# Kernel optimization log

Hardware: AMD Instinct MI355X
Metric: run time of the kernel (lower is better)

Reference implementation:

```python
import jax, jax.numpy as jnp
import numpy as np

B, NI, H, NC = 524288, 32, 128, 64


def _masks(ni, h):
    deg_in = jnp.arange(ni)                     # input layer: arange % ni == arange
    deg_hid = jnp.arange(h) % (ni - 1)
    deg_out = jnp.arange(2 * ni) % ni - 1
    m1 = (deg_hid[:, None] >= deg_in[None, :]).astype(jnp.float32)   # [H, NI]
    m2 = (deg_hid[:, None] >= deg_hid[None, :]).astype(jnp.float32)  # [H, H]
    m3 = (deg_out[:, None] >= deg_hid[None, :]).astype(jnp.float32)  # [2NI, H]
    return m1, m2, m3


def setup_inputs() -> dict:
    key = jax.random.key(0)
    ks = jax.random.split(key, 9)
    s = 0.05
    return {
        "x": jax.random.normal(ks[0], (B, NI), jnp.float32),
        "cond": jax.random.normal(ks[1], (B, NC), jnp.float32),
        "W1": jax.random.normal(ks[2], (H, NI), jnp.float32) * s,
        "b1": jnp.zeros((H,), jnp.float32),
        "Wc": jax.random.normal(ks[3], (H, NC), jnp.float32) * s,
        "W2": jax.random.normal(ks[4], (H, H), jnp.float32) * s,
        "b2": jnp.zeros((H,), jnp.float32),
        "W3": jax.random.normal(ks[5], (2 * NI, H), jnp.float32) * s,
        "b3": jnp.zeros((2 * NI,), jnp.float32),
    }


def reference(x, cond, W1, b1, Wc, W2, b2, W3, b3):
    ni = x.shape[1]
    h_dim = W1.shape[0]
    m1, m2, m3 = _masks(ni, h_dim)
    # joiner: masked linear + conditioning linear (no bias on cond)
    h = x @ (W1 * m1).T + b1 + cond @ Wc.T            # [B, H]
    h = jax.nn.relu(h)
    h = jax.nn.relu(h @ (W2 * m2).T + b2)             # [B, H]
    o = h @ (W3 * m3).T + b3                          # [B, 2NI]
    m_, a = o[:, :ni], o[:, ni:]
    a = jnp.clip(a, -5.0, 5.0)
    u = (x - m_) * jnp.exp(-a)
    logdet = -jnp.sum(a, axis=-1, keepdims=True)
    return u, logdet
```

## Files before the change

kernel.cpp:

```cpp
#include <hip/hip_runtime.h>


#define B_ROWS 524288
#define NI 32
#define HD 128
#define NC 64
#define ITERS 4

#define L2_BASE 24
#define L3_BASE 56
#define N_FRAGS 72

typedef _Float16 half8 __attribute__((ext_vector_type(8)));
typedef float f32x4 __attribute__((ext_vector_type(4)));

__device__ inline f32x4 relu4(f32x4 v) {
  v[0] = fmaxf(v[0], 0.f); v[1] = fmaxf(v[1], 0.f);
  v[2] = fmaxf(v[2], 0.f); v[3] = fmaxf(v[3], 0.f);
  return v;
}

__device__ inline half8 cvt8(f32x4 lo, f32x4 hi) {
  half8 h;
  h[0] = (_Float16)lo[0]; h[1] = (_Float16)lo[1];
  h[2] = (_Float16)lo[2]; h[3] = (_Float16)lo[3];
  h[4] = (_Float16)hi[0]; h[5] = (_Float16)hi[1];
  h[6] = (_Float16)hi[2]; h[7] = (_Float16)hi[3];
  return h;
}

__global__ void prep_weights(const float* __restrict__ W1, const float* __restrict__ Wc,
                             const float* __restrict__ W2, const float* __restrict__ W3,
                             _Float16* __restrict__ wf) {
  int tid = blockIdx.x * blockDim.x + threadIdx.x;
  if (tid >= N_FRAGS * 64) return;
  int frag = tid >> 6;
  int lane = tid & 63;
  int q = lane >> 4, c = lane & 15;
  int L, jt, kt;
  if (frag < L2_BASE)      { L = 0; jt = frag / 3;              kt = frag % 3; }
  else if (frag < L3_BASE) { L = 1; jt = (frag - L2_BASE) >> 2; kt = (frag - L2_BASE) & 3; }
  else                     { L = 2; jt = (frag - L3_BASE) >> 2; kt = (frag - L3_BASE) & 3; }
  int j = jt * 16 + c;
  half8 v;
#pragma unroll
  for (int e = 0; e < 8; ++e) {
    int k = kt * 32 + (e >> 2) * 16 + q * 4 + (e & 3);
    float w;
    if (L == 0) {
      if (k < NI) w = ((j % 31) >= k) ? W1[j * NI + k] : 0.f;
      else        w = Wc[j * NC + (k - NI)];
    } else if (L == 1) {
      w = ((j % 31) >= (k % 31)) ? W2[j * HD + k] : 0.f;
    } else {
      w = (((j % 32) - 1) >= (k % 31)) ? W3[j * HD + k] : 0.f;
    }
    v[e] = (_Float16)w;
  }
  *(half8*)(wf + (size_t)tid * 8) = v;
}


#define BODY(RX, RC, NRX, NRC, IT, SYNC)                                      \
  {                                                                           \
    half8 bf0 = cvt8(RX[0], RX[1]);                                           \
    half8 bf1 = cvt8(RC[0], RC[1]);                                           \
    half8 bf2 = cvt8(RC[2], RC[3]);                                           \
    if ((IT) < ITERS - 1) {     \
      long nr = blockBase + ((IT) + 1) * 128 + wid * 16 + c;                  \
      const f32x4* xr = (const f32x4*)(x + nr * NI);                          \
      const f32x4* cr = (const f32x4*)(cond + nr * NC);                       \
      NRX[0] = xr[q];     NRX[1] = xr[4 + q];                                 \
      NRC[0] = cr[q];     NRC[1] = cr[4 + q];                                 \
      NRC[2] = cr[8 + q]; NRC[3] = cr[12 + q];                                \
    }                                                                         \
    f32x4 acc[4]; half8 h1[4], h2[4];                                         \
          \
    _Pragma("unroll")                                                         \
    for (int jh = 0; jh < 2; ++jh) {                                          \
      _Pragma("unroll")                                                       \
      for (int j4 = 0; j4 < 4; ++j4)                                          \
        acc[j4] = *(const f32x4*)(b1 + (jh * 4 + j4) * 16 + q * 4);           \
      _Pragma("unroll")                                                       \
      for (int j4 = 0; j4 < 4; ++j4) {                                        \
        int jt = jh * 4 + j4;                                                 \
        _Pragma("unroll")                                                     \
        for (int kt = 0; kt < 3; ++kt) {                                      \
          half8 a = *(const half8*)(wf + (((jt * 3 + kt) * 64 + lane) << 3)); \
          half8 bb = (kt == 0) ? bf0 : ((kt == 1) ? bf1 : bf2);               \
          acc[j4] = __builtin_amdgcn_mfma_f32_16x16x32_f16(a, bb, acc[j4], 0, 0, 0); \
        }                                                                     \
      }                                                                       \
      _Pragma("unroll")                                                       \
      for (int p = 0; p < 2; ++p)                                             \
        h1[jh * 2 + p] = cvt8(relu4(acc[p * 2]), relu4(acc[p * 2 + 1]));      \
    }                                                                         \
    if (SYNC) __syncthreads();           \
                           \
    _Pragma("unroll")                                                         \
    for (int jh = 0; jh < 2; ++jh) {                                          \
      _Pragma("unroll")                                                       \
      for (int j4 = 0; j4 < 4; ++j4)                                          \
        acc[j4] = *(const f32x4*)(b2 + (jh * 4 + j4) * 16 + q * 4);           \
      _Pragma("unroll")                                                       \
      for (int j4 = 0; j4 < 4; ++j4) {                                        \
        int jt = jh * 4 + j4;                                                 \
        _Pragma("unroll")                                                     \
        for (int kt = 0; kt < 4; ++kt) {                                      \
          half8 a = *(const half8*)(wlds + (((jt * 4 + kt) * 64 + lane) << 3)); \
          acc[j4] = __builtin_amdgcn_mfma_f32_16x16x32_f16(a, h1[kt], acc[j4], 0, 0, 0); \
        }                                                                     \
      }                                                                       \
      _Pragma("unroll")                                                       \
      for (int p = 0; p < 2; ++p)                                             \
        h2[jh * 2 + p] = cvt8(relu4(acc[p * 2]), relu4(acc[p * 2 + 1]));      \
    }                                                                         \
                \
    _Pragma("unroll")                                                         \
    for (int jt = 0; jt < 4; ++jt)                                            \
      acc[jt] = *(const f32x4*)(b3 + jt * 16 + q * 4);                        \
    _Pragma("unroll")                                                         \
    for (int jt = 0; jt < 4; ++jt) {                                          \
      _Pragma("unroll")                                                       \
      for (int kt = 0; kt < 4; ++kt) {                                        \
        half8 a = *(const half8*)(wlds + (((32 + jt * 4 + kt) * 64 + lane) << 3)); \
        acc[jt] = __builtin_amdgcn_mfma_f32_16x16x32_f16(a, h2[kt], acc[jt], 0, 0, 0); \
      }                                                                       \
    }                                                                         \
                      \
    {                                                                         \
      long m = blockBase + (IT) * 128 + wid * 16 + c;                         \
      f32x4 xa = RX[0], xb = RX[1];                                           \
      f32x4 ua, ub;                                                           \
      float s = 0.f;                                                          \
      _Pragma("unroll")                                                       \
      for (int i = 0; i < 4; ++i) {                                           \
        float aa = fminf(fmaxf(acc[2][i], -5.f), 5.f);                        \
        float ab = fminf(fmaxf(acc[3][i], -5.f), 5.f);                        \
        ua[i] = (xa[i] - acc[0][i]) * __expf(-aa);                            \
        ub[i] = (xb[i] - acc[1][i]) * __expf(-ab);                            \
        s += aa + ab;                                                         \
      }                                                                       \
      *(f32x4*)(out + m * NI + q * 4) = ua;                                   \
      *(f32x4*)(out + m * NI + 16 + q * 4) = ub;                              \
      s += __shfl_xor(s, 16);                                                 \
      s += __shfl_xor(s, 32);                                                 \
      if (q == 0) out[(long)B_ROWS * NI + m] = -s;                            \
    }                                                                         \
  }

__global__ __launch_bounds__(512, 4) void made_fused(
    const float* __restrict__ x, const float* __restrict__ cond,
    const float* __restrict__ b1, const float* __restrict__ b2,
    const float* __restrict__ b3, const _Float16* __restrict__ wf,
    float* __restrict__ out) {
  __shared__ __align__(16) _Float16 wlds[48 * 512];

  const int tid  = threadIdx.x;
  const int lane = tid & 63;
  const int wid  = tid >> 6;
  const int q = lane >> 4, c = lane & 15;
  const long blockBase = (long)blockIdx.x * (ITERS * 128);

  f32x4 rxA[2], rcA[4], rxB[2], rcB[4];
  {
    long r = blockBase + wid * 16 + c;
    const f32x4* xr = (const f32x4*)(x + r * NI);
    const f32x4* cr = (const f32x4*)(cond + r * NC);
    rxA[0] = xr[q];     rxA[1] = xr[4 + q];
    rcA[0] = cr[q];     rcA[1] = cr[4 + q];
    rcA[2] = cr[8 + q]; rcA[3] = cr[12 + q];
  }

  {
    const char* gsrc = (const char*)(wf + L2_BASE * 512) + wid * 6144;
    char* ldst = (char*)wlds + wid * 6144;
#pragma unroll
    for (int i = 0; i < 6; ++i) {
      __builtin_amdgcn_global_load_lds(
          (const __attribute__((address_space(1))) void*)(gsrc + i * 1024 + lane * 16),
          (__attribute__((address_space(3))) void*)(ldst + i * 1024),
          16, 0, 0);
    }
  }

  BODY(rxA, rcA, rxB, rcB, 0, 1);
  BODY(rxB, rcB, rxA, rcA, 1, 0);
  BODY(rxA, rcA, rxB, rcB, 2, 0);
  BODY(rxB, rcB, rxA, rcA, 3, 0);
}

extern "C" void kernel_launch(void* const* d_in, const int* in_sizes, int n_in,
                              void* d_out, int out_size, void* d_ws, size_t ws_size,
                              hipStream_t stream) {
  const float* x    = (const float*)d_in[0];
  const float* cond = (const float*)d_in[1];
  const float* W1   = (const float*)d_in[2];
  const float* b1   = (const float*)d_in[3];
  const float* Wc   = (const float*)d_in[4];
  const float* W2   = (const float*)d_in[5];
  const float* b2   = (const float*)d_in[6];
  const float* W3   = (const float*)d_in[7];
  const float* b3   = (const float*)d_in[8];
  _Float16* wf = (_Float16*)d_ws;

  prep_weights<<<(N_FRAGS * 64 + 255) / 256, 256, 0, stream>>>(W1, Wc, W2, W3, wf);
  made_fused<<<B_ROWS / (ITERS * 128), 512, 0, stream>>>(x, cond, b1, b2, b3, wf, (float*)d_out);
}
```

Before: 313.5 us.

## Process two 16-row tiles per MFMA weight fragment with 256-thread blocks

Each wave now computes two 16-row column tiles per weight fragment load, so each A fragment (from global or LDS) feeds two MFMAs. Blocks shrink to 4 waves covering 256 rows, and each wave handles 64 rows in two halves, with the second half's inputs prefetched during layer 1 of the first. Each wave loads twice as much of the LDS weight block to make up for the fewer waves. The cost is roughly doubled accumulator and activation register use, and x for the second half is re-read from global memory in the epilogue; launch bounds drop to 3 blocks per CU.

```diff
diff --git a/kernel.cpp b/kernel.cpp
--- a/kernel.cpp
+++ b/kernel.cpp
@@ -5,7 +5,6 @@
 #define NI 32
 #define HD 128
 #define NC 64
-#define ITERS 4
 
 #define L2_BASE 24
 #define L3_BASE 56
@@ -60,96 +59,99 @@
   *(half8*)(wf + (size_t)tid * 8) = v;
 }
 
-
-#define BODY(RX, RC, NRX, NRC, IT, SYNC)                                      \
-  {                                                                           \
-    half8 bf0 = cvt8(RX[0], RX[1]);                                           \
-    half8 bf1 = cvt8(RC[0], RC[1]);                                           \
-    half8 bf2 = cvt8(RC[2], RC[3]);                                           \
-    if ((IT) < ITERS - 1) {     \
-      long nr = blockBase + ((IT) + 1) * 128 + wid * 16 + c;                  \
-      const f32x4* xr = (const f32x4*)(x + nr * NI);                          \
-      const f32x4* cr = (const f32x4*)(cond + nr * NC);                       \
-      NRX[0] = xr[q];     NRX[1] = xr[4 + q];                                 \
-      NRC[0] = cr[q];     NRC[1] = cr[4 + q];                                 \
-      NRC[2] = cr[8 + q]; NRC[3] = cr[12 + q];                                \
-    }                                                                         \
-    f32x4 acc[4]; half8 h1[4], h2[4];                                         \
-          \
-    _Pragma("unroll")                                                         \
-    for (int jh = 0; jh < 2; ++jh) {                                          \
-      _Pragma("unroll")                                                       \
-      for (int j4 = 0; j4 < 4; ++j4)                                          \
-        acc[j4] = *(const f32x4*)(b1 + (jh * 4 + j4) * 16 + q * 4);           \
-      _Pragma("unroll")                                                       \
-      for (int j4 = 0; j4 < 4; ++j4) {                                        \
-        int jt = jh * 4 + j4;                                                 \
+#define LAYER1(BF, H1)                                                        \
+  _Pragma("unroll")                                                           \
+  for (int jh = 0; jh < 2; ++jh) {                                            \
+    _Pragma("unroll")                                                         \
+    for (int j4 = 0; j4 < 4; ++j4) {                                          \
+      f32x4 bv = *(const f32x4*)(b1 + (jh * 4 + j4) * 16 + q * 4);            \
+      acc[j4][0] = bv; acc[j4][1] = bv;                                       \
+    }                                                                         \
+    _Pragma("unroll")                                                         \
+    for (int j4 = 0; j4 < 4; ++j4) {                                          \
+      int jt = jh * 4 + j4;                                                   \
+      _Pragma("unroll")                                                       \
+      for (int kt = 0; kt < 3; ++kt) {                                        \
+        half8 a = *(const half8*)(wf + (((jt * 3 + kt) * 64 + lane) << 3));   \
         _Pragma("unroll")                                                     \
-        for (int kt = 0; kt < 3; ++kt) {                                      \
-          half8 a = *(const half8*)(wf + (((jt * 3 + kt) * 64 + lane) << 3)); \
-          half8 bb = (kt == 0) ? bf0 : ((kt == 1) ? bf1 : bf2);               \
-          acc[j4] = __builtin_amdgcn_mfma_f32_16x16x32_f16(a, bb, acc[j4], 0, 0, 0); \
-        }                                                                     \
+        for (int nt = 0; nt < 2; ++nt)                                        \
+          acc[j4][nt] = __builtin_amdgcn_mfma_f32_16x16x32_f16(a, BF[kt][nt], acc[j4][nt], 0, 0, 0); \
       }                                                                       \
-      _Pragma("unroll")                                                       \
-      for (int p = 0; p < 2; ++p)                                             \
-        h1[jh * 2 + p] = cvt8(relu4(acc[p * 2]), relu4(acc[p * 2 + 1]));      \
-    }                                                                         \
-    if (SYNC) __syncthreads();           \
-                           \
-    _Pragma("unroll")                                                         \
-    for (int jh = 0; jh < 2; ++jh) {                                          \
-      _Pragma("unroll")                                                       \
-      for (int j4 = 0; j4 < 4; ++j4)                                          \
-        acc[j4] = *(const f32x4*)(b2 + (jh * 4 + j4) * 16 + q * 4);           \
-      _Pragma("unroll")                                                       \
-      for (int j4 = 0; j4 < 4; ++j4) {                                        \
-        int jt = jh * 4 + j4;                                                 \
+    }                                                                         \
+    _Pragma("unroll")                                                         \
+    for (int p = 0; p < 2; ++p)                                               \
+      _Pragma("unroll")                                                       \
+      for (int nt = 0; nt < 2; ++nt)                                          \
+        H1[jh * 2 + p][nt] = cvt8(relu4(acc[p * 2][nt]), relu4(acc[p * 2 + 1][nt])); \
+  }
+
+#define LAYER2(H1, H2)                                                        \
+  _Pragma("unroll")                                                           \
+  for (int jh = 0; jh < 2; ++jh) {                                            \
+    _Pragma("unroll")                                                         \
+    for (int j4 = 0; j4 < 4; ++j4) {                                          \
+      f32x4 bv = *(const f32x4*)(b2 + (jh * 4 + j4) * 16 + q * 4);            \
+      acc[j4][0] = bv; acc[j4][1] = bv;                                       \
+    }                                                                         \
+    _Pragma("unroll")                                                         \
+    for (int j4 = 0; j4 < 4; ++j4) {                                          \
+      int jt = jh * 4 + j4;                                                   \
+      _Pragma("unroll")                                                       \
+      for (int kt = 0; kt < 4; ++kt) {                                        \
+        half8 a = *(const half8*)(wlds + (((jt * 4 + kt) * 64 + lane) << 3)); \
         _Pragma("unroll")                                                     \
-        for (int kt = 0; kt < 4; ++kt) {                                      \
-          half8 a = *(const half8*)(wlds + (((jt * 4 + kt) * 64 + lane) << 3)); \
-          acc[j4] = __builtin_amdgcn_mfma_f32_16x16x32_f16(a, h1[kt], acc[j4], 0, 0, 0); \
-        }                                                                     \
+        for (int nt = 0; nt < 2; ++nt)                                        \
+          acc[j4][nt] = __builtin_amdgcn_mfma_f32_16x16x32_f16(a, H1[kt][nt], acc[j4][nt], 0, 0, 0); \
       }                                                                       \
-      _Pragma("unroll")                                                       \
-      for (int p = 0; p < 2; ++p)                                             \
-        h2[jh * 2 + p] = cvt8(relu4(acc[p * 2]), relu4(acc[p * 2 + 1]));      \
-    }                                                                         \
-                \
-    _Pragma("unroll")                                                         \
-    for (int jt = 0; jt < 4; ++jt)                                            \
-      acc[jt] = *(const f32x4*)(b3 + jt * 16 + q * 4);                        \
-    _Pragma("unroll")                                                         \
-    for (int jt = 0; jt < 4; ++jt) {                                          \
-      _Pragma("unroll")                                                       \
-      for (int kt = 0; kt < 4; ++kt) {                                        \
-        half8 a = *(const half8*)(wlds + (((32 + jt * 4 + kt) * 64 + lane) << 3)); \
-        acc[jt] = __builtin_amdgcn_mfma_f32_16x16x32_f16(a, h2[kt], acc[jt], 0, 0, 0); \
-      }                                                                       \
-    }                                                                         \
-                      \
-    {                                                                         \
-      long m = blockBase + (IT) * 128 + wid * 16 + c;                         \
-      f32x4 xa = RX[0], xb = RX[1];                                           \
-      f32x4 ua, ub;                                                           \
-      float s = 0.f;                                                          \
-      _Pragma("unroll")                                                       \
-      for (int i = 0; i < 4; ++i) {                                           \
-        float aa = fminf(fmaxf(acc[2][i], -5.f), 5.f);                        \
-        float ab = fminf(fmaxf(acc[3][i], -5.f), 5.f);                        \
-        ua[i] = (xa[i] - acc[0][i]) * __expf(-aa);                            \
-        ub[i] = (xb[i] - acc[1][i]) * __expf(-ab);                            \
-        s += aa + ab;                                                         \
-      }                                                                       \
-      *(f32x4*)(out + m * NI + q * 4) = ua;                                   \
-      *(f32x4*)(out + m * NI + 16 + q * 4) = ub;                              \
-      s += __shfl_xor(s, 16);                                                 \
-      s += __shfl_xor(s, 32);                                                 \
-      if (q == 0) out[(long)B_ROWS * NI + m] = -s;                            \
-    }                                                                         \
-  }
-
-__global__ __launch_bounds__(512, 4) void made_fused(
+    }                                                                         \
+    _Pragma("unroll")                                                         \
+    for (int p = 0; p < 2; ++p)                                               \
+      _Pragma("unroll")                                                       \
+      for (int nt = 0; nt < 2; ++nt)                                          \
+        H2[jh * 2 + p][nt] = cvt8(relu4(acc[p * 2][nt]), relu4(acc[p * 2 + 1][nt])); \
+  }
+
+#define LAYER3(H2)                                                            \
+  _Pragma("unroll")                                                           \
+  for (int jt = 0; jt < 4; ++jt) {                                            \
+    f32x4 bv = *(const f32x4*)(b3 + jt * 16 + q * 4);                         \
+    acc[jt][0] = bv; acc[jt][1] = bv;                                         \
+  }                                                                           \
+  _Pragma("unroll")                                                           \
+  for (int jt = 0; jt < 4; ++jt)                                              \
+    _Pragma("unroll")                                                         \
+    for (int kt = 0; kt < 4; ++kt) {                                          \
+      half8 a = *(const half8*)(wlds + (((32 + jt * 4 + kt) * 64 + lane) << 3)); \
+      _Pragma("unroll")                                                       \
+      for (int nt = 0; nt < 2; ++nt)                                          \
+        acc[jt][nt] = __builtin_amdgcn_mfma_f32_16x16x32_f16(a, H2[kt][nt], acc[jt][nt], 0, 0, 0); \
+    }
+
+#define EPILOGUE(TILEROW, XA, XB)                                             \
+  _Pragma("unroll")                                                           \
+  for (int nt = 0; nt < 2; ++nt) {                                            \
+    long m = (TILEROW) + nt * 16 + c;                                         \
+    f32x4 xa = XA, xb = XB;                                                   \
+    f32x4 mva = acc[0][nt], mvb = acc[1][nt];                                 \
+    f32x4 ava = acc[2][nt], avb = acc[3][nt];                                 \
+    f32x4 ua, ub;                                                             \
+    float s = 0.f;                                                            \
+    _Pragma("unroll")                                                         \
+    for (int i = 0; i < 4; ++i) {                                             \
+      float aa = fminf(fmaxf(ava[i], -5.f), 5.f);                             \
+      float ab = fminf(fmaxf(avb[i], -5.f), 5.f);                             \
+      ua[i] = (xa[i] - mva[i]) * __expf(-aa);                                 \
+      ub[i] = (xb[i] - mvb[i]) * __expf(-ab);                                 \
+      s += aa + ab;                                                           \
+    }                                                                         \
+    *(f32x4*)(out + m * NI + q * 4) = ua;                                     \
+    *(f32x4*)(out + m * NI + 16 + q * 4) = ub;                                \
+    s += __shfl_xor(s, 16);                                                   \
+    s += __shfl_xor(s, 32);                                                   \
+    if (q == 0) out[(long)B_ROWS * NI + m] = -s;                              \
+  }
+
+__global__ __launch_bounds__(256, 3) void made_fused(
     const float* __restrict__ x, const float* __restrict__ cond,
     const float* __restrict__ b1, const float* __restrict__ b2,
     const float* __restrict__ b3, const _Float16* __restrict__ wf,
@@ -160,23 +162,23 @@
   const int lane = tid & 63;
   const int wid  = tid >> 6;
   const int q = lane >> 4, c = lane & 15;
-  const long blockBase = (long)blockIdx.x * (ITERS * 128);
-
-  f32x4 rxA[2], rcA[4], rxB[2], rcB[4];
+  const long waveRow = ((long)blockIdx.x * 4 + wid) * 64;
+
+  f32x4 xv0[2][2], cv0[2][4];
+#pragma unroll
+  for (int nt = 0; nt < 2; ++nt) {
+    const f32x4* xr = (const f32x4*)(x    + (waveRow + nt * 16 + c) * NI);
+    const f32x4* cr = (const f32x4*)(cond + (waveRow + nt * 16 + c) * NC);
+    xv0[nt][0] = xr[q];     xv0[nt][1] = xr[4 + q];
+    cv0[nt][0] = cr[q];     cv0[nt][1] = cr[4 + q];
+    cv0[nt][2] = cr[8 + q]; cv0[nt][3] = cr[12 + q];
+  }
+
   {
-    long r = blockBase + wid * 16 + c;
-    const f32x4* xr = (const f32x4*)(x + r * NI);
-    const f32x4* cr = (const f32x4*)(cond + r * NC);
-    rxA[0] = xr[q];     rxA[1] = xr[4 + q];
-    rcA[0] = cr[q];     rcA[1] = cr[4 + q];
-    rcA[2] = cr[8 + q]; rcA[3] = cr[12 + q];
-  }
-
-  {
-    const char* gsrc = (const char*)(wf + L2_BASE * 512) + wid * 6144;
-    char* ldst = (char*)wlds + wid * 6144;
-#pragma unroll
-    for (int i = 0; i < 6; ++i) {
+    const char* gsrc = (const char*)(wf + L2_BASE * 512) + wid * 12288;
+    char* ldst = (char*)wlds + wid * 12288;
+#pragma unroll
+    for (int i = 0; i < 12; ++i) {
       __builtin_amdgcn_global_load_lds(
           (const __attribute__((address_space(1))) void*)(gsrc + i * 1024 + lane * 16),
           (__attribute__((address_space(3))) void*)(ldst + i * 1024),
@@ -184,10 +186,49 @@
     }
   }
 
-  BODY(rxA, rcA, rxB, rcB, 0, 1);
-  BODY(rxB, rcB, rxA, rcA, 1, 0);
-  BODY(rxA, rcA, rxB, rcB, 2, 0);
-  BODY(rxB, rcB, rxA, rcA, 3, 0);
+  half8 bf0[3][2];
+#pragma unroll
+  for (int nt = 0; nt < 2; ++nt) {
+    bf0[0][nt] = cvt8(xv0[nt][0], xv0[nt][1]);
+    bf0[1][nt] = cvt8(cv0[nt][0], cv0[nt][1]);
+    bf0[2][nt] = cvt8(cv0[nt][2], cv0[nt][3]);
+  }
+
+  f32x4 xv1[2][2], cv1[2][4];
+#pragma unroll
+  for (int nt = 0; nt < 2; ++nt) {
+    const f32x4* xr = (const f32x4*)(x    + (waveRow + 32 + nt * 16 + c) * NI);
+    const f32x4* cr = (const f32x4*)(cond + (waveRow + 32 + nt * 16 + c) * NC);
+    xv1[nt][0] = xr[q];     xv1[nt][1] = xr[4 + q];
+    cv1[nt][0] = cr[q];     cv1[nt][1] = cr[4 + q];
+    cv1[nt][2] = cr[8 + q]; cv1[nt][3] = cr[12 + q];
+  }
+
+  f32x4 acc[4][2];
+  half8 h1[4][2], h2[4][2];
+
+  LAYER1(bf0, h1);
+
+  half8 bf1[3][2];
+#pragma unroll
+  for (int nt = 0; nt < 2; ++nt) {
+    bf1[0][nt] = cvt8(xv1[nt][0], xv1[nt][1]);
+    bf1[1][nt] = cvt8(cv1[nt][0], cv1[nt][1]);
+    bf1[2][nt] = cvt8(cv1[nt][2], cv1[nt][3]);
+  }
+
+  __syncthreads();
+
+  LAYER2(h1, h2);
+  LAYER3(h2);
+  EPILOGUE(waveRow, xv0[nt][0], xv0[nt][1]);
+
+  LAYER1(bf1, h1);
+  LAYER2(h1, h2);
+  LAYER3(h2);
+  EPILOGUE(waveRow + 32,
+           (*(const f32x4*)(x + (waveRow + 32 + nt * 16 + c) * NI + q * 4)),
+           (*(const f32x4*)(x + (waveRow + 32 + nt * 16 + c) * NI + 16 + q * 4)));
 }
 
 extern "C" void kernel_launch(void* const* d_in, const int* in_sizes, int n_in,
@@ -205,5 +246,5 @@
   _Float16* wf = (_Float16*)d_ws;
 
   prep_weights<<<(N_FRAGS * 64 + 255) / 256, 256, 0, stream>>>(W1, Wc, W2, W3, wf);
-  made_fused<<<B_ROWS / (ITERS * 128), 512, 0, stream>>>(x, cond, b1, b2, b3, wf, (float*)d_out);
-}
+  made_fused<<<B_ROWS / 256, 256, 0, stream>>>(x, cond, b1, b2, b3, wf, (float*)d_out);
+}
```

After: 304.3 us. -2.9%, faster.
